# Optimization experiments

Hardware: AMD Instinct MI355X
Metric: run time of the kernel (lower is better)

Reference implementation:

```python
import jax, jax.numpy as jnp
import numpy as np

BS, N, C, KNN = 2, 65536, 256, 16

def setup_inputs() -> dict:
    key = jax.random.key(0)
    ks = jax.random.split(key, 8)
    s = 1.0 / np.sqrt(C)
    return {
        "Q": jax.random.normal(ks[0], (BS, N, C), jnp.float32),
        "K": jax.random.normal(ks[1], (BS, N, C), jnp.float32),
        "V": jax.random.normal(ks[2], (BS, N, C), jnp.float32),
        "knn_idx": jax.random.randint(ks[3], (N, KNN), 0, N, jnp.int32),
        "Wq_w": jax.random.normal(ks[4], (C, C), jnp.float32) * s,
        "Wq_b": jnp.zeros((C,), jnp.float32),
        "Wk_w": jax.random.normal(ks[5], (C, C), jnp.float32) * s,
        "Wk_b": jnp.zeros((C,), jnp.float32),
        "Wv_w": jax.random.normal(ks[6], (C, C), jnp.float32) * s,
        "Wv_b": jnp.zeros((C,), jnp.float32),
        "ln_g": jnp.ones((C,), jnp.float32),
        "ln_b": jnp.zeros((C,), jnp.float32),
    }

def _layernorm(x, g, b, eps=1e-5):
    mu = jnp.mean(x, axis=-1, keepdims=True)
    var = jnp.mean(jnp.square(x - mu), axis=-1, keepdims=True)
    return (x - mu) * jax.lax.rsqrt(var + eps) * g + b

def reference(Q, K, V, knn_idx, Wq_w, Wq_b, Wk_w, Wk_b, Wv_w, Wv_b, ln_g, ln_b):
    c = Q.shape[-1]
    # torch nn.Linear: x @ W.T + b
    Qp = Q @ Wq_w.T + Wq_b                     # (bs, N, C)
    Kp = K @ Wk_w.T + Wk_b
    Vp = V @ Wv_w.T + Wv_b
    K_knn = Kp[:, knn_idx, :]                  # (bs, N, k, C) gather over node dim
    V_knn = Vp[:, knn_idx, :]
    attn = jnp.einsum('bnc,bnkc->bnk', Qp, K_knn) / jnp.sqrt(jnp.asarray(c, Qp.dtype))
    attn = jax.nn.softmax(attn, axis=-1)       # (bs, N, k)
    out = jnp.einsum('bnk,bnkc->bnc', attn, V_knn)
    return _layernorm(out + Qp, ln_g, ln_b)
```

## Files before the change

kernel.cpp:

```cpp
#include <hip/hip_runtime.h>

#define BS 2
#define NN 65536
#define CC 256
#define KNNK 16

typedef short bf16x8 __attribute__((ext_vector_type(8)));
typedef float f32x4 __attribute__((ext_vector_type(4)));

__device__ __forceinline__ unsigned f2bf(float f) {
  unsigned u = __builtin_bit_cast(unsigned, f);
  return (u + 0x7FFFu + ((u >> 16) & 1u)) >> 16;
}
__device__ __forceinline__ int pack2(float a, float b) {
  return (int)(f2bf(a) | (f2bf(b) << 16));
}
__device__ __forceinline__ float bfu(unsigned short v) {
  return __builtin_bit_cast(float, ((unsigned)v) << 16);
}
__device__ __forceinline__ float bflo(unsigned u) { return __builtin_bit_cast(float, u << 16); }
__device__ __forceinline__ float bfhi(unsigned u) { return __builtin_bit_cast(float, u & 0xFFFF0000u); }

template <int OUT_BF16>
__global__ __launch_bounds__(512)
void proj_kernel(const float* __restrict__ A, const float* __restrict__ W,
                 const float* __restrict__ bias, void* __restrict__ Out) {
  constexpr int K = 256, TM = 128, LDS_S = 40;
  __shared__ __align__(16) unsigned short As[TM * LDS_S];
  __shared__ __align__(16) unsigned short Bs[256 * LDS_S];
  const int t = threadIdx.x;
  const int wave = t >> 6;
  const int lane = t & 63;
  const int wm = wave >> 2, wn = wave & 3;
  const int lrow = lane & 15, quad = lane >> 4;
  const long row0 = (long)blockIdx.x * TM;

  const int ar = t >> 2, akb = t & 3;
  const int br = t >> 1, bkb = t & 1;
  const float* aptr = A + (row0 + ar) * K + akb * 8;
  const float* bptr = W + (long)br * K + bkb * 16;

  f32x4 acc[4][4];
#pragma unroll
  for (int i = 0; i < 4; ++i)
#pragma unroll
    for (int j = 0; j < 4; ++j) acc[i][j] = f32x4{0.f, 0.f, 0.f, 0.f};

  for (int k0 = 0; k0 < K; k0 += 32) {
    float4 a0 = *(const float4*)(aptr + k0);
    float4 a1 = *(const float4*)(aptr + k0 + 4);
    float4 b0 = *(const float4*)(bptr + k0);
    float4 b1 = *(const float4*)(bptr + k0 + 4);
    float4 b2 = *(const float4*)(bptr + k0 + 8);
    float4 b3 = *(const float4*)(bptr + k0 + 12);
    __syncthreads();
    *(int4*)&As[ar * LDS_S + akb * 8] =
        make_int4(pack2(a0.x, a0.y), pack2(a0.z, a0.w), pack2(a1.x, a1.y), pack2(a1.z, a1.w));
    *(int4*)&Bs[br * LDS_S + bkb * 16] =
        make_int4(pack2(b0.x, b0.y), pack2(b0.z, b0.w), pack2(b1.x, b1.y), pack2(b1.z, b1.w));
    *(int4*)&Bs[br * LDS_S + bkb * 16 + 8] =
        make_int4(pack2(b2.x, b2.y), pack2(b2.z, b2.w), pack2(b3.x, b3.y), pack2(b3.z, b3.w));
    __syncthreads();
    bf16x8 af[4], bfr[4];
#pragma unroll
    for (int mi = 0; mi < 4; ++mi)
      af[mi] = *(const bf16x8*)&As[(wm * 64 + mi * 16 + lrow) * LDS_S + quad * 8];
#pragma unroll
    for (int ni = 0; ni < 4; ++ni)
      bfr[ni] = *(const bf16x8*)&Bs[(wn * 64 + ni * 16 + lrow) * LDS_S + quad * 8];
#pragma unroll
    for (int mi = 0; mi < 4; ++mi)
#pragma unroll
      for (int ni = 0; ni < 4; ++ni)
        acc[mi][ni] = __builtin_amdgcn_mfma_f32_16x16x32_bf16(af[mi], bfr[ni], acc[mi][ni], 0, 0, 0);
  }

#pragma unroll
  for (int mi = 0; mi < 4; ++mi)
#pragma unroll
    for (int ni = 0; ni < 4; ++ni) {
      const long gr0 = row0 + wm * 64 + mi * 16 + quad * 4;
      const int gc = wn * 64 + ni * 16 + lrow;
      const float bv = bias[gc];
#pragma unroll
      for (int r = 0; r < 4; ++r) {
        float v = acc[mi][ni][r] + bv;
        if (OUT_BF16)
          ((unsigned short*)Out)[(gr0 + r) * 256 + gc] = (unsigned short)f2bf(v);
        else
          ((float*)Out)[(gr0 + r) * 256 + gc] = v;
      }
    }
}

__global__ __launch_bounds__(256)
void attn_kernel(const float* __restrict__ Qp, const unsigned short* __restrict__ Kp,
                 const unsigned short* __restrict__ Vp, const int* __restrict__ knn,
                 const float* __restrict__ ln_g, const float* __restrict__ ln_b,
                 float* __restrict__ out) {
  const int n = blockIdx.x, b = blockIdx.y, t = threadIdx.x;
  __shared__ int sidx[KNNK];
  __shared__ float sdots[KNNK];
  __shared__ float sred[8];
  if (t < KNNK) sidx[t] = knn[n * KNNK + t];
  __syncthreads();

  const long base = ((long)b * NN + n) * CC;
  const long kbase = (long)b * NN * CC;
  int nbr[KNNK];
#pragma unroll
  for (int i = 0; i < KNNK; ++i) nbr[i] = sidx[i];

  const int k = t >> 4, cg = t & 15;
  {
    const float* qp = Qp + base + cg * 16;
    float4 q0 = *(const float4*)(qp);
    float4 q1 = *(const float4*)(qp + 4);
    float4 q2 = *(const float4*)(qp + 8);
    float4 q3 = *(const float4*)(qp + 12);
    const unsigned short* kr = Kp + kbase + (long)nbr[k] * CC + cg * 16;
    int4 kv0 = *(const int4*)(kr);
    int4 kv1 = *(const int4*)(kr + 8);
    float p = q0.x * bflo(kv0.x) + q0.y * bfhi(kv0.x)
            + q0.z * bflo(kv0.y) + q0.w * bfhi(kv0.y)
            + q1.x * bflo(kv0.z) + q1.y * bfhi(kv0.z)
            + q1.z * bflo(kv0.w) + q1.w * bfhi(kv0.w)
            + q2.x * bflo(kv1.x) + q2.y * bfhi(kv1.x)
            + q2.z * bflo(kv1.y) + q2.w * bfhi(kv1.y)
            + q3.x * bflo(kv1.z) + q3.y * bfhi(kv1.z)
            + q3.z * bflo(kv1.w) + q3.w * bfhi(kv1.w);
#pragma unroll
    for (int m = 1; m < 16; m <<= 1) p += __shfl_xor(p, m);
    if (cg == 0) sdots[k] = p * 0.0625f;
  }
  __syncthreads();

  float d[KNNK];
#pragma unroll
  for (int i = 0; i < KNNK; ++i) d[i] = sdots[i];
  float mx = d[0];
#pragma unroll
  for (int i = 1; i < KNNK; ++i) mx = fmaxf(mx, d[i]);
  float s = 0.f;
#pragma unroll
  for (int i = 0; i < KNNK; ++i) { d[i] = __expf(d[i] - mx); s += d[i]; }
  const float inv = 1.0f / s;

  float o = 0.f;
#pragma unroll
  for (int i = 0; i < KNNK; ++i)
    o += d[i] * bfu(Vp[kbase + (long)nbr[i] * CC + t]);
  o *= inv;
  o += Qp[base + t];

  float s1 = o, s2 = o * o;
#pragma unroll
  for (int m = 1; m < 64; m <<= 1) {
    s1 += __shfl_xor(s1, m);
    s2 += __shfl_xor(s2, m);
  }
  const int wv = t >> 6;
  if ((t & 63) == 0) { sred[wv] = s1; sred[wv + 4] = s2; }
  __syncthreads();
  const float S1 = sred[0] + sred[1] + sred[2] + sred[3];
  const float S2 = sred[4] + sred[5] + sred[6] + sred[7];
  const float mu = S1 * (1.0f / 256.0f);
  const float var = S2 * (1.0f / 256.0f) - mu * mu;
  const float rs = rsqrtf(var + 1e-5f);
  out[base + t] = (o - mu) * rs * ln_g[t] + ln_b[t];
}

extern "C" void kernel_launch(void* const* d_in, const int* in_sizes, int n_in,
                              void* d_out, int out_size, void* d_ws, size_t ws_size,
                              hipStream_t stream) {
  const float* Q   = (const float*)d_in[0];
  const float* K   = (const float*)d_in[1];
  const float* V   = (const float*)d_in[2];
  const int*   knn = (const int*)d_in[3];
  const float* Wq  = (const float*)d_in[4];
  const float* Wqb = (const float*)d_in[5];
  const float* Wk  = (const float*)d_in[6];
  const float* Wkb = (const float*)d_in[7];
  const float* Wv  = (const float*)d_in[8];
  const float* Wvb = (const float*)d_in[9];
  const float* ln_g = (const float*)d_in[10];
  const float* ln_b = (const float*)d_in[11];
  float* out = (float*)d_out;

  float* Qp = (float*)d_ws;
  unsigned short* Kp = (unsigned short*)((char*)d_ws + (size_t)BS * NN * CC * 4);
  unsigned short* Vp = Kp + (size_t)BS * NN * CC;

  proj_kernel<0><<<1024, 512, 0, stream>>>(Q, Wq, Wqb, (void*)Qp);
  proj_kernel<1><<<1024, 512, 0, stream>>>(K, Wk, Wkb, (void*)Kp);
  proj_kernel<1><<<1024, 512, 0, stream>>>(V, Wv, Wvb, (void*)Vp);
  attn_kernel<<<dim3(NN, BS), 256, 0, stream>>>(Qp, Kp, Vp, knn, ln_g, ln_b, out);
}
```

Before: 799.3 us.

## Merge QKV projections into one kernel with direct-to-LDS loads and pre-converted bf16 weights

Weights are converted to bf16 once in a small kernel, staged temporarily in the output buffer. The three projection GEMMs are merged into one launch that uses global_load_lds for both operands, with an XOR-swizzled fp32 A tile and 64-row tiles. The A tile is converted to bf16 when read from LDS. The attention kernel now computes the softmax with 16 threads and shuffles instead of every thread redundantly. The goal is to remove the register round-trip and per-element conversion on the load path and cut launch count, at the cost of a smaller M tile and a single-buffered loop.

```diff
diff --git a/kernel.cpp b/kernel.cpp
--- a/kernel.cpp
+++ b/kernel.cpp
@@ -1,4 +1,5 @@
 #include <hip/hip_runtime.h>
+#include <hip/hip_bf16.h>
 
 #define BS 2
 #define NN 65536
@@ -7,88 +8,126 @@
 
 typedef short bf16x8 __attribute__((ext_vector_type(8)));
 typedef float f32x4 __attribute__((ext_vector_type(4)));
-
-__device__ __forceinline__ unsigned f2bf(float f) {
-  unsigned u = __builtin_bit_cast(unsigned, f);
-  return (u + 0x7FFFu + ((u >> 16) & 1u)) >> 16;
-}
-__device__ __forceinline__ int pack2(float a, float b) {
-  return (int)(f2bf(a) | (f2bf(b) << 16));
-}
+typedef int i32x4 __attribute__((ext_vector_type(4)));
+
 __device__ __forceinline__ float bfu(unsigned short v) {
   return __builtin_bit_cast(float, ((unsigned)v) << 16);
 }
 __device__ __forceinline__ float bflo(unsigned u) { return __builtin_bit_cast(float, u << 16); }
 __device__ __forceinline__ float bfhi(unsigned u) { return __builtin_bit_cast(float, u & 0xFFFF0000u); }
 
-template <int OUT_BF16>
-__global__ __launch_bounds__(512)
-void proj_kernel(const float* __restrict__ A, const float* __restrict__ W,
-                 const float* __restrict__ bias, void* __restrict__ Out) {
-  constexpr int K = 256, TM = 128, LDS_S = 40;
-  __shared__ __align__(16) unsigned short As[TM * LDS_S];
-  __shared__ __align__(16) unsigned short Bs[256 * LDS_S];
+__device__ __forceinline__ void gl16(const void* g, void* l) {
+  __builtin_amdgcn_global_load_lds((const __attribute__((address_space(1))) void*)g,
+                                   (__attribute__((address_space(3))) void*)l, 16, 0, 0);
+}
+
+__device__ __forceinline__ int pk2(float a, float b) {
+  union { __hip_bfloat162 h; int i; } u;
+  u.h = __float22bfloat162_rn(make_float2(a, b));
+  return u.i;
+}
+__device__ __forceinline__ bf16x8 cvt8(f32x4 a, f32x4 b) {
+  i32x4 p;
+  p[0] = pk2(a[0], a[1]);
+  p[1] = pk2(a[2], a[3]);
+  p[2] = pk2(b[0], b[1]);
+  p[3] = pk2(b[2], b[3]);
+  return __builtin_bit_cast(bf16x8, p);
+}
+__device__ __forceinline__ unsigned short f2b(float f) {
+  union { __hip_bfloat16 h; unsigned short s; } u;
+  u.h = __float2bfloat16(f);
+  return u.s;
+}
+
+__global__ __launch_bounds__(256)
+void convw_kernel(const float* __restrict__ Wq, const float* __restrict__ Wk,
+                  const float* __restrict__ Wv, unsigned short* __restrict__ W16) {
+  const float* src = (blockIdx.y == 0) ? Wq : (blockIdx.y == 1) ? Wk : Wv;
+  unsigned short* dst = W16 + blockIdx.y * 65536;
+  const int i = (blockIdx.x * 256 + threadIdx.x) * 4;
+  float4 v = *(const float4*)(src + i);
+  *(int2*)(dst + i) = make_int2(pk2(v.x, v.y), pk2(v.z, v.w));
+}
+
+__global__ __launch_bounds__(256)
+void proj3_kernel(const float* __restrict__ Qin, const float* __restrict__ Kin,
+                  const float* __restrict__ Vin, const unsigned short* __restrict__ W16,
+                  const float* __restrict__ Qb, const float* __restrict__ Kb,
+                  const float* __restrict__ Vb,
+                  float* __restrict__ Qp, unsigned short* __restrict__ Kp,
+                  unsigned short* __restrict__ Vp) {
+  constexpr int BK = 32;
+  __shared__ __align__(16) float As[64 * BK];
+  __shared__ __align__(16) unsigned short Bsh[256 * BK];
+
+  const int z = blockIdx.y;
+  const float* A = (z == 0) ? Qin : (z == 1) ? Kin : Vin;
+  const unsigned short* W = W16 + z * 65536;
+  const float* bias = (z == 0) ? Qb : (z == 1) ? Kb : Vb;
+
   const int t = threadIdx.x;
-  const int wave = t >> 6;
-  const int lane = t & 63;
-  const int wm = wave >> 2, wn = wave & 3;
-  const int lrow = lane & 15, quad = lane >> 4;
-  const long row0 = (long)blockIdx.x * TM;
-
-  const int ar = t >> 2, akb = t & 3;
-  const int br = t >> 1, bkb = t & 1;
-  const float* aptr = A + (row0 + ar) * K + akb * 8;
-  const float* bptr = W + (long)br * K + bkb * 16;
-
-  f32x4 acc[4][4];
-#pragma unroll
-  for (int i = 0; i < 4; ++i)
-#pragma unroll
-    for (int j = 0; j < 4; ++j) acc[i][j] = f32x4{0.f, 0.f, 0.f, 0.f};
-
-  for (int k0 = 0; k0 < K; k0 += 32) {
-    float4 a0 = *(const float4*)(aptr + k0);
-    float4 a1 = *(const float4*)(aptr + k0 + 4);
-    float4 b0 = *(const float4*)(bptr + k0);
-    float4 b1 = *(const float4*)(bptr + k0 + 4);
-    float4 b2 = *(const float4*)(bptr + k0 + 8);
-    float4 b3 = *(const float4*)(bptr + k0 + 12);
+  const int w = t >> 6, l = t & 63;
+  const int lrow = l & 15, quad = l >> 4;
+  const int wm = w >> 1, wn = w & 1;
+  const long row0 = (long)blockIdx.x * 64;
+
+  const float* aS = A + (row0 + w * 16 + (l >> 3)) * 256 + (((l & 7) ^ (l >> 3)) << 2);
+  const unsigned short* bS = W + (w * 64 + (l >> 2)) * 256 + ((l & 3) << 3);
+  float* ldsA0 = &As[(w * 16) * BK];
+  float* ldsA1 = &As[(w * 16 + 8) * BK];
+  unsigned short* ldsB0 = &Bsh[(w * 64) * BK];
+
+  const int xA = lrow & 7;
+  const float* ra0 = &As[(wm * 32 + lrow) * BK + (((2 * quad) ^ xA) << 2)];
+  const float* ra1 = &As[(wm * 32 + lrow) * BK + (((2 * quad + 1) ^ xA) << 2)];
+  const unsigned short* rb = &Bsh[(wn * 128 + lrow) * BK + quad * 8];
+
+  f32x4 acc[2][8];
+#pragma unroll
+  for (int i = 0; i < 2; ++i)
+#pragma unroll
+    for (int j = 0; j < 8; ++j) acc[i][j] = f32x4{0.f, 0.f, 0.f, 0.f};
+
+  for (int k0 = 0; k0 < 256; k0 += BK) {
+    gl16(aS + k0, ldsA0);
+    gl16(aS + k0 + 8 * 256, ldsA1);
+    gl16(bS + k0, ldsB0);
+    gl16(bS + k0 + 1 * 16 * 256, ldsB0 + 1 * 16 * BK);
+    gl16(bS + k0 + 2 * 16 * 256, ldsB0 + 2 * 16 * BK);
+    gl16(bS + k0 + 3 * 16 * 256, ldsB0 + 3 * 16 * BK);
     __syncthreads();
-    *(int4*)&As[ar * LDS_S + akb * 8] =
-        make_int4(pack2(a0.x, a0.y), pack2(a0.z, a0.w), pack2(a1.x, a1.y), pack2(a1.z, a1.w));
-    *(int4*)&Bs[br * LDS_S + bkb * 16] =
-        make_int4(pack2(b0.x, b0.y), pack2(b0.z, b0.w), pack2(b1.x, b1.y), pack2(b1.z, b1.w));
-    *(int4*)&Bs[br * LDS_S + bkb * 16 + 8] =
-        make_int4(pack2(b2.x, b2.y), pack2(b2.z, b2.w), pack2(b3.x, b3.y), pack2(b3.z, b3.w));
+    bf16x8 af[2], bfr[8];
+#pragma unroll
+    for (int mi = 0; mi < 2; ++mi) {
+      f32x4 f0 = *(const f32x4*)(ra0 + mi * 16 * BK);
+      f32x4 f1 = *(const f32x4*)(ra1 + mi * 16 * BK);
+      af[mi] = cvt8(f0, f1);
+    }
+#pragma unroll
+    for (int ni = 0; ni < 8; ++ni) bfr[ni] = *(const bf16x8*)(rb + ni * 16 * BK);
+#pragma unroll
+    for (int mi = 0; mi < 2; ++mi)
+#pragma unroll
+      for (int ni = 0; ni < 8; ++ni)
+        acc[mi][ni] = __builtin_amdgcn_mfma_f32_16x16x32_bf16(af[mi], bfr[ni], acc[mi][ni], 0, 0, 0);
     __syncthreads();
-    bf16x8 af[4], bfr[4];
-#pragma unroll
-    for (int mi = 0; mi < 4; ++mi)
-      af[mi] = *(const bf16x8*)&As[(wm * 64 + mi * 16 + lrow) * LDS_S + quad * 8];
-#pragma unroll
-    for (int ni = 0; ni < 4; ++ni)
-      bfr[ni] = *(const bf16x8*)&Bs[(wn * 64 + ni * 16 + lrow) * LDS_S + quad * 8];
-#pragma unroll
-    for (int mi = 0; mi < 4; ++mi)
-#pragma unroll
-      for (int ni = 0; ni < 4; ++ni)
-        acc[mi][ni] = __builtin_amdgcn_mfma_f32_16x16x32_bf16(af[mi], bfr[ni], acc[mi][ni], 0, 0, 0);
-  }
-
-#pragma unroll
-  for (int mi = 0; mi < 4; ++mi)
-#pragma unroll
-    for (int ni = 0; ni < 4; ++ni) {
-      const long gr0 = row0 + wm * 64 + mi * 16 + quad * 4;
-      const int gc = wn * 64 + ni * 16 + lrow;
+  }
+
+#pragma unroll
+  for (int mi = 0; mi < 2; ++mi)
+#pragma unroll
+    for (int ni = 0; ni < 8; ++ni) {
+      const long gr0 = row0 + wm * 32 + mi * 16 + quad * 4;
+      const int gc = wn * 128 + ni * 16 + lrow;
       const float bv = bias[gc];
-#pragma unroll
-      for (int r = 0; r < 4; ++r) {
-        float v = acc[mi][ni][r] + bv;
-        if (OUT_BF16)
-          ((unsigned short*)Out)[(gr0 + r) * 256 + gc] = (unsigned short)f2bf(v);
-        else
-          ((float*)Out)[(gr0 + r) * 256 + gc] = v;
+      if (z == 0) {
+#pragma unroll
+        for (int r = 0; r < 4; ++r) Qp[(gr0 + r) * 256 + gc] = acc[mi][ni][r] + bv;
+      } else {
+        unsigned short* O = (z == 1) ? Kp : Vp;
+#pragma unroll
+        for (int r = 0; r < 4; ++r) O[(gr0 + r) * 256 + gc] = f2b(acc[mi][ni][r] + bv);
       }
     }
 }
@@ -101,6 +140,7 @@
   const int n = blockIdx.x, b = blockIdx.y, t = threadIdx.x;
   __shared__ int sidx[KNNK];
   __shared__ float sdots[KNNK];
+  __shared__ float sw[KNNK];
   __shared__ float sred[8];
   if (t < KNNK) sidx[t] = knn[n * KNNK + t];
   __syncthreads();
@@ -135,22 +175,26 @@
   }
   __syncthreads();
 
-  float d[KNNK];
-#pragma unroll
-  for (int i = 0; i < KNNK; ++i) d[i] = sdots[i];
-  float mx = d[0];
-#pragma unroll
-  for (int i = 1; i < KNNK; ++i) mx = fmaxf(mx, d[i]);
-  float s = 0.f;
-#pragma unroll
-  for (int i = 0; i < KNNK; ++i) { d[i] = __expf(d[i] - mx); s += d[i]; }
-  const float inv = 1.0f / s;
-
+  if (t < KNNK) {
+    float v = sdots[t];
+    float mx = v;
+#pragma unroll
+    for (int m = 1; m < 16; m <<= 1) mx = fmaxf(mx, __shfl_xor(mx, m));
+    float e = __expf(v - mx);
+    float s = e;
+#pragma unroll
+    for (int m = 1; m < 16; m <<= 1) s += __shfl_xor(s, m);
+    sw[t] = e / s;
+  }
+  __syncthreads();
+
+  float wgt[KNNK];
+#pragma unroll
+  for (int i = 0; i < KNNK; ++i) wgt[i] = sw[i];
   float o = 0.f;
 #pragma unroll
   for (int i = 0; i < KNNK; ++i)
-    o += d[i] * bfu(Vp[kbase + (long)nbr[i] * CC + t]);
-  o *= inv;
+    o += wgt[i] * bfu(Vp[kbase + (long)nbr[i] * CC + t]);
   o += Qp[base + t];
 
   float s1 = o, s2 = o * o;
@@ -190,9 +234,9 @@
   float* Qp = (float*)d_ws;
   unsigned short* Kp = (unsigned short*)((char*)d_ws + (size_t)BS * NN * CC * 4);
   unsigned short* Vp = Kp + (size_t)BS * NN * CC;
-
-  proj_kernel<0><<<1024, 512, 0, stream>>>(Q, Wq, Wqb, (void*)Qp);
-  proj_kernel<1><<<1024, 512, 0, stream>>>(K, Wk, Wkb, (void*)Kp);
-  proj_kernel<1><<<1024, 512, 0, stream>>>(V, Wv, Wvb, (void*)Vp);
+  unsigned short* W16 = (unsigned short*)d_out;
+
+  convw_kernel<<<dim3(64, 3), 256, 0, stream>>>(Wq, Wk, Wv, W16);
+  proj3_kernel<<<dim3(2048, 3), 256, 0, stream>>>(Q, K, V, W16, Wqb, Wkb, Wvb, Qp, Kp, Vp);
   attn_kernel<<<dim3(NN, BS), 256, 0, stream>>>(Qp, Kp, Vp, knn, ln_g, ln_b, out);
 }
```

Result: no change. 785.8 us (-1.7%).
